# Optimization experiments

Measured on AMD Instinct MI355X. Metric: run time of the kernel, lower is better.

## Reference

```python
import jax, jax.numpy as jnp
from jax import lax
import numpy as np

IMG = 2048.0            # square image size (W=H)
STRIDES = [32, 64, 128]
FEATS = [64, 32, 16]    # IMG / stride
NUM_CLASSES = 80
BATCH = 8
SCORE_THRESH = 0.2
NMS_THRESH = 0.6
TOPK = 1000             # topk_candidates per level
DETS = 100              # detections_per_img


def make_anchors(fs, stride):
    # square anchors of size==stride centered on the feature grid (AnchorGenerator with ratio 1.0)
    c = (jnp.arange(fs, dtype=jnp.float32) + 0.5) * stride
    cy, cx = jnp.meshgrid(c, c, indexing='ij')
    cx, cy = cx.reshape(-1), cy.reshape(-1)
    h = stride / 2.0
    return jnp.stack([cx - h, cy - h, cx + h, cy + h], axis=1)


def setup_inputs() -> dict:
    key = jax.random.key(0)
    inp = {}
    for i, (fs, s) in enumerate(zip(FEATS, STRIDES)):
        hw = fs * fs
        key, k1, k2, k3 = jax.random.split(key, 4)
        inp[f'cls{i}'] = jax.random.normal(k1, (BATCH, hw, NUM_CLASSES), jnp.float32)
        inp[f'reg{i}'] = jax.random.uniform(k2, (BATCH, hw, 4), jnp.float32)
        inp[f'ctr{i}'] = jax.random.normal(k3, (BATCH, hw), jnp.float32)
        inp[f'anc{i}'] = make_anchors(fs, float(s))
    return inp


def _decode(rel, boxes):
    # BoxLinearCoder.decode_single with normalize_by_size=True
    cx = 0.5 * (boxes[:, 0] + boxes[:, 2])
    cy = 0.5 * (boxes[:, 1] + boxes[:, 3])
    w = boxes[:, 2] - boxes[:, 0]
    h = boxes[:, 3] - boxes[:, 1]
    rel = rel * jnp.stack([w, h, w, h], axis=1)
    return jnp.stack([cx - rel[:, 0], cy - rel[:, 1], cx + rel[:, 2], cy + rel[:, 3]], axis=1)


def _iou(b):
    # torchvision box_iou on a single set of boxes [N,4] -> [N,N]
    area = (b[:, 2] - b[:, 0]) * (b[:, 3] - b[:, 1])
    lt = jnp.maximum(b[:, None, :2], b[None, :, :2])
    rb = jnp.minimum(b[:, None, 2:], b[None, :, 2:])
    wh = jnp.clip(rb - lt, 0.0)
    inter = wh[..., 0] * wh[..., 1]
    return inter / (area[:, None] + area[None, :] - inter)


def _greedy_keep(iou):
    # classic greedy NMS on score-sorted boxes: suppress j>i with iou>thresh if i kept
    n = iou.shape[0]
    idx = jnp.arange(n)
    def body(i, keep):
        supp = keep[i] & (iou[i] > NMS_THRESH) & (idx > i)
        return keep & ~supp
    return lax.fori_loop(0, n, body, jnp.ones((n,), bool))


def _per_image(cls_l, reg_l, ctr_l, anc_l):
    boxes, scores, labels = [], [], []
    for cls, reg, ctr, anc in zip(cls_l, reg_l, ctr_l, anc_l):
        hw, c = cls.shape
        # scores = sqrt(sigmoid(cls) * sigmoid(ctrness)) flattened over anchors*classes
        sc = jnp.sqrt(jax.nn.sigmoid(cls) * jax.nn.sigmoid(ctr)[:, None]).reshape(-1)
        sc = jnp.where(sc > SCORE_THRESH, sc, -1.0)  # score threshold as mask (static shapes)
        ts, ti = lax.top_k(sc, TOPK)                 # per-level top-k candidates
        aidx = ti // c
        lab = ti % c
        b = jnp.clip(_decode(reg[aidx], anc[aidx]), 0.0, IMG)  # decode + clip to image
        boxes.append(b); scores.append(ts); labels.append(lab)
    boxes = jnp.concatenate(boxes)    # [3*TOPK, 4]
    scores = jnp.concatenate(scores)  # [3*TOPK]
    labels = jnp.concatenate(labels)  # [3*TOPK]
    n = scores.shape[0]
    # batched_nms via per-class coordinate offsets
    off = labels.astype(boxes.dtype) * (IMG + 1.0)
    ss, oi = lax.top_k(scores, n)     # sort candidates by score desc
    bs = boxes[oi] + off[oi][:, None]
    keep = lax.stop_gradient(_greedy_keep(_iou(bs)))
    fsc = jnp.where(keep & (ss > 0), ss, -1.0)
    fs, fi = lax.top_k(fsc, DETS)     # keep detections_per_img; score==-1 marks padding
    return boxes[oi][fi], fs, labels[oi][fi]


def reference(cls0, cls1, cls2, reg0, reg1, reg2, ctr0, ctr1, ctr2, anc0, anc1, anc2):
    f = jax.vmap(lambda c0, c1, c2, r0, r1, r2, t0, t1, t2: _per_image(
        [c0, c1, c2], [r0, r1, r2], [t0, t1, t2], [anc0, anc1, anc2]))
    return f(cls0, cls1, cls2, reg0, reg1, reg2, ctr0, ctr1, ctr2)
```

## Files before the change

### kernel.cpp

```cpp
#include <hip/hip_runtime.h>

#define NCLS  80
#define TOPK  384
#define SELK  512
#define NLVL  3
#define NIMG  8
#define NCAND (NLVL * TOPK)
#define DETS  100
#define CAP   1024
#define HBINS 4096
#define NHBLK 16
#define NCBLK 64
#define QBASE 0x3F800000u
#define QMAX  0x41C80000u
#define IMGSZ 2048.0f


__device__ __forceinline__ float sigm(float x) {
    if (x >= 0.f) return 1.f / (1.f + expf(-x));
    float e = expf(x);
    return e / (1.f + e);
}

__device__ __forceinline__ unsigned int qbits(float ea, float t1) {
    return __float_as_uint(__fmul_rn(__fadd_rn(1.f, ea), t1));
}

__device__ __forceinline__ void bitonic_desc(unsigned long long* s, int N) {
    for (int k = 2; k <= N; k <<= 1) {
        for (int j = k >> 1; j > 0; j >>= 1) {
            __syncthreads();
            for (int i = threadIdx.x; i < N; i += blockDim.x) {
                int ixj = i ^ j;
                if (ixj > i) {
                    unsigned long long a = s[i], b = s[ixj];
                    bool up = ((i & k) == 0);
                    if (up ? (a < b) : (a > b)) { s[i] = b; s[ixj] = a; }
                }
            }
        }
    }
    __syncthreads();
}

__device__ __forceinline__ void lvl_select(int level,
    const float* c0, const float* c1, const float* c2,
    const float* t0, const float* t1, const float* t2,
    const float** cls, const float** ctr, int* hw) {
    if (level == 0)      { *cls = c0; *ctr = t0; *hw = 4096; }
    else if (level == 1) { *cls = c1; *ctr = t1; *hw = 1024; }
    else                 { *cls = c2; *ctr = t2; *hw = 256; }
}


__global__ void k_hist(const float* c0, const float* c1, const float* c2,
                       const float* t0, const float* t1, const float* t2,
                       unsigned int* parts, unsigned int* counters) {
    int level = blockIdx.z, img = blockIdx.y;
    int pair = img * NLVL + level;
    if (blockIdx.x == 0 && threadIdx.x == 0) counters[pair * 16] = 0;
    const float* cls; const float* ctr; int hw;
    lvl_select(level, c0, c1, c2, t0, t1, t2, &cls, &ctr, &hw);
    int n4 = hw * (NCLS / 4);
    const float4* cl4 = (const float4*)(cls + (size_t)img * hw * NCLS);
    const float* ct = ctr + (size_t)img * hw;
    __shared__ unsigned int h[HBINS];
    for (int i = threadIdx.x; i < HBINS; i += 256) h[i] = 0;
    __syncthreads();
    for (int i = blockIdx.x * 256 + threadIdx.x; i < n4; i += NHBLK * 256) {
        float4 v = cl4[i];
        int a = i / (NCLS / 4);
        float eb = expf(-ct[a]);
        float t1 = __fadd_rn(1.f, eb);
        #pragma unroll
        for (int k = 0; k < 4; ++k) {
            float x = (k == 0) ? v.x : (k == 1) ? v.y : (k == 2) ? v.z : v.w;
            unsigned int qb = qbits(expf(-x), t1);
            if (qb < QMAX) {
                unsigned int bin = (qb - QBASE) >> 13;
                if (bin > HBINS - 1) bin = HBINS - 1;
                atomicAdd(&h[bin], 1u);
            }
        }
    }
    __syncthreads();
    unsigned int* P = parts + ((size_t)(pair * NHBLK + blockIdx.x)) * HBINS;
    for (int i = threadIdx.x; i < HBINS; i += 256) P[i] = h[i];
}


__global__ void k_find(const unsigned int* parts, unsigned int* vcut) {
    int pair = blockIdx.x;
    int tid = threadIdx.x;
    __shared__ unsigned int hb[HBINS];
    __shared__ unsigned int segsum[256];
    __shared__ unsigned int pref[256];
    unsigned int acc[HBINS / 256];
    #pragma unroll
    for (int j = 0; j < HBINS / 256; ++j) acc[j] = 0;
    for (int blk = 0; blk < NHBLK; ++blk) {
        const unsigned int* P = parts + ((size_t)(pair * NHBLK + blk)) * HBINS;
        #pragma unroll
        for (int j = 0; j < HBINS / 256; ++j) acc[j] += P[tid + 256 * j];
    }
    #pragma unroll
    for (int j = 0; j < HBINS / 256; ++j) hb[tid + 256 * j] = acc[j];
    __syncthreads();
    unsigned int seg = 0;
    #pragma unroll
    for (int j = 0; j < 16; ++j) seg += hb[16 * tid + j];
    segsum[tid] = seg;
    pref[tid] = seg;
    __syncthreads();
    for (int off = 1; off < 256; off <<= 1) {
        unsigned int v = (tid >= off) ? pref[tid - off] : 0u;
        __syncthreads();
        pref[tid] += v;
        __syncthreads();
    }
    unsigned int incl = pref[tid];
    unsigned int excl = incl - seg;
    if (excl < (unsigned int)SELK && incl >= (unsigned int)SELK) {
        unsigned int cum = excl; int B = HBINS - 1;
        for (int b = 16 * tid; b < 16 * tid + 16; ++b) {
            cum += hb[b];
            if (cum >= (unsigned int)SELK) { B = b; break; }
        }
        vcut[pair] = (B >= HBINS - 1) ? QMAX : (QBASE + ((unsigned int)(B + 1) << 13));
    }
    if (tid == 255 && pref[255] < (unsigned int)SELK)
        vcut[pair] = QMAX;
}


__global__ void k_collect(const float* c0, const float* c1, const float* c2,
                          const float* t0, const float* t1, const float* t2,
                          const unsigned int* vcut, unsigned int* counters,
                          unsigned long long* buf) {
    int level = blockIdx.z, img = blockIdx.y;
    const float* cls; const float* ctr; int hw;
    lvl_select(level, c0, c1, c2, t0, t1, t2, &cls, &ctr, &hw);
    int n4 = hw * (NCLS / 4);
    int pair = img * NLVL + level;
    const float4* cl4 = (const float4*)(cls + (size_t)img * hw * NCLS);
    const float* ct = ctr + (size_t)img * hw;
    unsigned int V = vcut[pair];
    __shared__ unsigned long long sbuf[CAP];
    __shared__ unsigned int scnt;
    __shared__ unsigned int sbase;
    if (threadIdx.x == 0) scnt = 0;
    __syncthreads();
    for (int i = blockIdx.x * 256 + threadIdx.x; i < n4; i += NCBLK * 256) {
        float4 v = cl4[i];
        int a = i / (NCLS / 4);
        float cta = ct[a];
        float eb = expf(-cta);
        float t1 = __fadd_rn(1.f, eb);
        #pragma unroll
        for (int k = 0; k < 4; ++k) {
            float x = (k == 0) ? v.x : (k == 1) ? v.y : (k == 2) ? v.z : v.w;
            unsigned int qb = qbits(expf(-x), t1);
            if (qb < V) {
                float s = sqrtf(sigm(x) * sigm(cta));
                unsigned int e = (unsigned int)(4 * i + k);
                unsigned int slot = atomicAdd(&scnt, 1u);
                if (slot < CAP)
                    sbuf[slot] = ((unsigned long long)__float_as_uint(s) << 32) | (~e);
            }
        }
    }
    __syncthreads();
    unsigned int cl_n = scnt; if (cl_n > CAP) cl_n = CAP;
    if (threadIdx.x == 0)
        sbase = atomicAdd(&counters[pair * 16], cl_n);
    __syncthreads();
    unsigned int base = sbase;
    for (unsigned int idx = threadIdx.x; idx < cl_n; idx += 256) {
        unsigned int g = base + idx;
        if (g < CAP) buf[(size_t)pair * CAP + g] = sbuf[idx];
    }
}


__global__ void __launch_bounds__(1024)
k_sort_pairs(const unsigned long long* buf, const unsigned int* counters,
             const float* r0, const float* r1, const float* r2,
             const float* a0, const float* a1, const float* a2,
             float* cand_box, int* cand_lab, unsigned long long* gkey) {
    int pair = blockIdx.x;
    int img = pair / NLVL, level = pair % NLVL;
    __shared__ unsigned long long s[CAP];
    int cnt = (int)counters[pair * 16]; if (cnt > CAP) cnt = CAP;
    for (int i = threadIdx.x; i < CAP; i += 1024)
        s[i] = (i < cnt) ? buf[(size_t)pair * CAP + i] : 0ull;
    bitonic_desc(s, CAP);
    const float* reg; const float* anc; int hw;
    if (level == 0)      { reg = r0; anc = a0; hw = 4096; }
    else if (level == 1) { reg = r1; anc = a1; hw = 1024; }
    else                 { reg = r2; anc = a2; hw = 256; }
    const float* rg = reg + (size_t)img * hw * 4;
    for (int r = threadIdx.x; r < TOPK; r += 1024) {
        unsigned long long key = s[r];
        int cpos = level * TOPK + r;
        size_t o = (size_t)img * NCAND + cpos;
        float b0 = 0, b1 = 0, b2 = 0, b3 = 0; int lab = 0; unsigned int bits = 0;
        if (key != 0ull) {
            bits = (unsigned int)(key >> 32);
            unsigned int idx = ~((unsigned int)key);
            int a = (int)(idx / NCLS); lab = (int)(idx % NCLS);
            float ax1 = anc[a * 4 + 0], ay1 = anc[a * 4 + 1];
            float ax2 = anc[a * 4 + 2], ay2 = anc[a * 4 + 3];
            float cx = 0.5f * (ax1 + ax2), cy = 0.5f * (ay1 + ay2);
            float w = ax2 - ax1, h = ay2 - ay1;
            float e0 = rg[a * 4 + 0] * w, e1 = rg[a * 4 + 1] * h;
            float e2 = rg[a * 4 + 2] * w, e3 = rg[a * 4 + 3] * h;
            b0 = fminf(fmaxf(cx - e0, 0.f), IMGSZ);
            b1 = fminf(fmaxf(cy - e1, 0.f), IMGSZ);
            b2 = fminf(fmaxf(cx + e2, 0.f), IMGSZ);
            b3 = fminf(fmaxf(cy + e3, 0.f), IMGSZ);
        }
        cand_box[o * 4 + 0] = b0; cand_box[o * 4 + 1] = b1;
        cand_box[o * 4 + 2] = b2; cand_box[o * 4 + 3] = b3;
        cand_lab[o] = lab;
        gkey[o] = ((unsigned long long)bits << 32) | (unsigned int)(~((unsigned int)cpos));
    }
}


__global__ void __launch_bounds__(1024)
k_merge_nms(const unsigned long long* gkey, const float* cand_box, const int* cand_lab,
            float* out) {
    int img = blockIdx.x;
    int tid = threadIdx.x;
    __shared__ unsigned long long A[TOPK], B[TOPK], C[TOPK];
    __shared__ unsigned long long M[2 * TOPK];
    __shared__ unsigned long long S[NCAND];
    __shared__ float4 wbox[NCAND];
    __shared__ int    wlab[NCAND];
    __shared__ float4 sbx[64]; __shared__ float sar[64];
    __shared__ float4 koff[DETS]; __shared__ float karr[DETS];
    __shared__ float4 kb[DETS]; __shared__ float ks[DETS]; __shared__ int kl[DETS];
    __shared__ float4 rb[DETS]; __shared__ int rl[DETS];

    const unsigned long long* G = gkey + (size_t)img * NCAND;
    for (int i = tid; i < TOPK; i += 1024) { A[i] = G[i]; B[i] = G[TOPK + i]; C[i] = G[2 * TOPK + i]; }
    __syncthreads();

    for (int k = tid; k < 2 * TOPK; k += 1024) {
        int lo = max(0, k - TOPK), hi = min(k, TOPK);
        while (lo < hi) {
            int mid = (lo + hi) >> 1;
            if (A[mid] > B[k - mid - 1]) lo = mid + 1; else hi = mid;
        }
        int i = lo, j = k - lo;
        unsigned long long av = (i < TOPK) ? A[i] : 0ull;
        unsigned long long bv = (j < TOPK) ? B[j] : 0ull;
        M[k] = (av > bv) ? av : bv;
    }
    __syncthreads();
    for (int k = tid; k < NCAND; k += 1024) {
        int lo = max(0, k - TOPK), hi = min(k, 2 * TOPK);
        while (lo < hi) {
            int mid = (lo + hi) >> 1;
            if (M[mid] > C[k - mid - 1]) lo = mid + 1; else hi = mid;
        }
        int i = lo, j = k - lo;
        unsigned long long mv = (i < 2 * TOPK) ? M[i] : 0ull;
        unsigned long long cv = (j < TOPK) ? C[j] : 0ull;
        S[k] = (mv > cv) ? mv : cv;
    }
    __syncthreads();

    const float4* CB4 = (const float4*)cand_box + (size_t)img * NCAND;
    const int* CL = cand_lab + (size_t)img * NCAND;
    for (int i = tid; i < NCAND; i += 1024) {
        unsigned int pos = ~((unsigned int)S[i]);
        float4 b4 = make_float4(0.f, 0.f, 0.f, 0.f); int lbv = 0;
        if (pos < NCAND) { b4 = CB4[pos]; lbv = CL[pos]; }
        wbox[i] = b4; wlab[i] = lbv;
    }
    __syncthreads();

    if (tid >= 64) return;
    int lane = tid;
    unsigned long long lmask_lt = (lane == 0) ? 0ull : (~0ull >> (64 - lane));

    int kept = 0, ring = 0, r = 0;

    while (kept < DETS && r < NCAND) {
        int rank = r + lane;
        unsigned long long key = (rank < NCAND) ? S[rank] : 0ull;
        unsigned int bits = (unsigned int)(key >> 32);
        unsigned long long pm = __ballot(bits != 0u);
        int npos = (pm == ~0ull) ? 64 : (int)__builtin_ctzll(~pm);
        if (npos == 0) break;

        float4 bx = make_float4(0.f, 0.f, 0.f, 0.f); int lb = 0;
        if (lane < npos) { bx = wbox[rank]; lb = wlab[rank]; }
        float off = (float)lb * (IMGSZ + 1.0f);
        float ox1 = bx.x + off, oy1 = bx.y + off;
        float ox2 = bx.z + off, oy2 = bx.w + off;
        float car = (ox2 - ox1) * (oy2 - oy1);
        sbx[lane] = make_float4(ox1, oy1, ox2, oy2);
        sar[lane] = car;

        bool supk = false;
        for (int k2 = 0; k2 < kept; ++k2) {
            float4 kk = koff[k2]; float ka = karr[k2];
            float lx = fmaxf(kk.x, ox1), ly = fmaxf(kk.y, oy1);
            float rx = fminf(kk.z, ox2), ry = fminf(kk.w, oy2);
            float w = fmaxf(rx - lx, 0.f), h = fmaxf(ry - ly, 0.f);
            float inter = w * h;
            supk = supk || (inter / (ka + car - inter) > 0.6f);
        }
        unsigned long long col = 0ull;
        for (int i = 0; i < npos; ++i) {
            float4 c = sbx[i]; float ca = sar[i];
            float lx = fmaxf(c.x, ox1), ly = fmaxf(c.y, oy1);
            float rx = fminf(c.z, ox2), ry = fminf(c.w, oy2);
            float w = fmaxf(rx - lx, 0.f), h = fmaxf(ry - ly, 0.f);
            float inter = w * h;
            if ((inter / (ca + car - inter) > 0.6f) && (i < lane)) col |= (1ull << i);
        }
        unsigned long long undecided = __ballot((lane < npos) && !supk);
        unsigned long long aliveSel = 0ull;
        int capleft = DETS - kept;
        int lastSlot = npos - 1;
        while (undecided) {
            int i = (int)__builtin_ctzll(undecided);
            aliveSel |= (1ull << i);
            undecided &= ~(1ull << i);
            if (--capleft == 0) { lastSlot = i; break; }
            unsigned long long row = __ballot(((col >> i) & 1ull) != 0ull);
            undecided &= ~row;
        }
        unsigned long long region = (lastSlot >= 63) ? ~0ull : ((1ull << (lastSlot + 1)) - 1ull);
        region &= (npos >= 64) ? ~0ull : ((1ull << npos) - 1ull);
        unsigned long long rejm = region & ~aliveSel;

        if ((aliveSel >> lane) & 1ull) {
            int ki = kept + (int)__popcll(aliveSel & lmask_lt);
            koff[ki] = make_float4(ox1, oy1, ox2, oy2); karr[ki] = car;
            kb[ki] = bx; ks[ki] = __uint_as_float(bits); kl[ki] = lb;
        }
        if ((rejm >> lane) & 1ull) {
            int ri = ring + (int)__popcll(rejm & lmask_lt);
            if (ri < DETS) { rb[ri] = bx; rl[ri] = lb; }
        }
        kept += (int)__popcll(aliveSel);
        ring += (int)__popcll(rejm);
        r += lastSlot + 1;
    }

    while (kept < DETS && ring < DETS && r < NCAND) {
        int rank = r + lane;
        if (rank < NCAND) {
            int ri = ring + lane;
            if (ri < DETS) { rb[ri] = wbox[rank]; rl[ri] = wlab[rank]; }
        }
        int take = NCAND - r; if (take > 64) take = 64;
        ring += take;
        r += 64;
    }

    for (int k = lane; k < DETS; k += 64) {
        float4 bxo; float scv; int lv;
        if (k < kept) { bxo = kb[k]; scv = ks[k]; lv = kl[k]; }
        else { int q = k - kept; bxo = rb[q]; scv = -1.0f; lv = rl[q]; }
        float* ob = out + ((size_t)img * DETS + k) * 4;
        ob[0] = bxo.x; ob[1] = bxo.y; ob[2] = bxo.z; ob[3] = bxo.w;
        out[NIMG * DETS * 4 + img * DETS + k] = scv;
        out[NIMG * DETS * 5 + img * DETS + k] = (float)lv;
    }
}


extern "C" void kernel_launch(void* const* d_in, const int* in_sizes, int n_in,
                              void* d_out, int out_size, void* d_ws, size_t ws_size,
                              hipStream_t stream) {
    (void)in_sizes; (void)n_in; (void)out_size; (void)ws_size;
    const float* cls0 = (const float*)d_in[0];
    const float* reg0 = (const float*)d_in[1];
    const float* ctr0 = (const float*)d_in[2];
    const float* anc0 = (const float*)d_in[3];
    const float* cls1 = (const float*)d_in[4];
    const float* reg1 = (const float*)d_in[5];
    const float* ctr1 = (const float*)d_in[6];
    const float* anc1 = (const float*)d_in[7];
    const float* cls2 = (const float*)d_in[8];
    const float* reg2 = (const float*)d_in[9];
    const float* ctr2 = (const float*)d_in[10];
    const float* anc2 = (const float*)d_in[11];
    float* out = (float*)d_out;
    char* ws = (char*)d_ws;

    const size_t OFF_PARTS = 0;
    const size_t OFF_CNT   = 6291456;
    const size_t OFF_VCUT  = 6292992;
    const size_t OFF_BUF   = 6293120;
    const size_t OFF_CBOX  = 6489728;
    const size_t OFF_CLAB  = 6637184;
    const size_t OFF_GKEY  = 6674048;

    unsigned int* parts = (unsigned int*)(ws + OFF_PARTS);
    unsigned int* cnt   = (unsigned int*)(ws + OFF_CNT);
    unsigned int* vcut  = (unsigned int*)(ws + OFF_VCUT);
    unsigned long long* buf  = (unsigned long long*)(ws + OFF_BUF);
    float* cand_box = (float*)(ws + OFF_CBOX);
    int*   cand_lab = (int*)(ws + OFF_CLAB);
    unsigned long long* gkey = (unsigned long long*)(ws + OFF_GKEY);

    k_hist<<<dim3(NHBLK, NIMG, NLVL), 256, 0, stream>>>(
        cls0, cls1, cls2, ctr0, ctr1, ctr2, parts, cnt);
    k_find<<<24, 256, 0, stream>>>(parts, vcut);
    k_collect<<<dim3(NCBLK, NIMG, NLVL), 256, 0, stream>>>(
        cls0, cls1, cls2, ctr0, ctr1, ctr2, vcut, cnt, buf);
    k_sort_pairs<<<24, 1024, 0, stream>>>(buf, cnt, reg0, reg1, reg2, anc0, anc1, anc2,
                                          cand_box, cand_lab, gkey);
    k_merge_nms<<<NIMG, 1024, 0, stream>>>(gkey, cand_box, cand_lab, out);
}
```

Before: 160.7 us.

## Fuse per-level sort and cross-level merge into one image-wide bitonic sort

Removes the separate per-(image,level) sort kernel and the global candidate staging buffers. The merge kernel now loads all three levels' collected keys for an image into a 4096-entry shared array, bitonic-sorts them together, and decodes boxes for the top 1024. The level is encoded into the key payload so decoding can recover it. This saves one launch and the global round trip plus merge-path searches, but runs a larger sort on only 8 blocks and changes the candidate set semantics from per-level top-k to global top-1024.

```diff
diff --git a/kernel.cpp b/kernel.cpp
--- a/kernel.cpp
+++ b/kernel.cpp
@@ -1,13 +1,13 @@
 #include <hip/hip_runtime.h>
 
 #define NCLS  80
-#define TOPK  384
 #define SELK  512
 #define NLVL  3
 #define NIMG  8
-#define NCAND (NLVL * TOPK)
 #define DETS  100
 #define CAP   1024
+#define NSORT 4096
+#define NDEC  1024
 #define HBINS 4096
 #define NHBLK 16
 #define NCBLK 64
@@ -163,9 +163,10 @@
             if (qb < V) {
                 float s = sqrtf(sigm(x) * sigm(cta));
                 unsigned int e = (unsigned int)(4 * i + k);
+                unsigned int p = ((unsigned int)level << 19) | e;
                 unsigned int slot = atomicAdd(&scnt, 1u);
                 if (slot < CAP)
-                    sbuf[slot] = ((unsigned long long)__float_as_uint(s) << 32) | (~e);
+                    sbuf[slot] = ((unsigned long long)__float_as_uint(s) << 32) | (~p);
             }
         }
     }
@@ -183,101 +184,55 @@
 
 
 __global__ void __launch_bounds__(1024)
-k_sort_pairs(const unsigned long long* buf, const unsigned int* counters,
-             const float* r0, const float* r1, const float* r2,
-             const float* a0, const float* a1, const float* a2,
-             float* cand_box, int* cand_lab, unsigned long long* gkey) {
-    int pair = blockIdx.x;
-    int img = pair / NLVL, level = pair % NLVL;
-    __shared__ unsigned long long s[CAP];
-    int cnt = (int)counters[pair * 16]; if (cnt > CAP) cnt = CAP;
-    for (int i = threadIdx.x; i < CAP; i += 1024)
-        s[i] = (i < cnt) ? buf[(size_t)pair * CAP + i] : 0ull;
-    bitonic_desc(s, CAP);
-    const float* reg; const float* anc; int hw;
-    if (level == 0)      { reg = r0; anc = a0; hw = 4096; }
-    else if (level == 1) { reg = r1; anc = a1; hw = 1024; }
-    else                 { reg = r2; anc = a2; hw = 256; }
-    const float* rg = reg + (size_t)img * hw * 4;
-    for (int r = threadIdx.x; r < TOPK; r += 1024) {
-        unsigned long long key = s[r];
-        int cpos = level * TOPK + r;
-        size_t o = (size_t)img * NCAND + cpos;
-        float b0 = 0, b1 = 0, b2 = 0, b3 = 0; int lab = 0; unsigned int bits = 0;
+k_merge_nms(const unsigned long long* buf, const unsigned int* counters,
+            const float* r0, const float* r1, const float* r2,
+            const float* a0, const float* a1, const float* a2,
+            float* out) {
+    int img = blockIdx.x;
+    int tid = threadIdx.x;
+    __shared__ unsigned long long S[NSORT];
+    __shared__ float4 wbox[NDEC];
+    __shared__ int    wlab[NDEC];
+    __shared__ float4 sbx[64]; __shared__ float sar[64];
+    __shared__ float4 koff[DETS]; __shared__ float karr[DETS];
+    __shared__ float4 kb[DETS]; __shared__ float ks[DETS]; __shared__ int kl[DETS];
+    __shared__ float4 rb[DETS]; __shared__ int rl[DETS];
+
+    for (int l = 0; l < NLVL; ++l) {
+        int pair = img * NLVL + l;
+        int c = (int)counters[pair * 16]; if (c > CAP) c = CAP;
+        const unsigned long long* B = buf + (size_t)pair * CAP;
+        for (int i = tid; i < CAP; i += 1024)
+            S[l * CAP + i] = (i < c) ? B[i] : 0ull;
+    }
+    for (int i = NLVL * CAP + tid; i < NSORT; i += 1024) S[i] = 0ull;
+    bitonic_desc(S, NSORT);
+
+    {
+        unsigned long long key = S[tid];
+        float4 b4 = make_float4(0.f, 0.f, 0.f, 0.f); int lbv = 0;
         if (key != 0ull) {
-            bits = (unsigned int)(key >> 32);
-            unsigned int idx = ~((unsigned int)key);
-            int a = (int)(idx / NCLS); lab = (int)(idx % NCLS);
+            unsigned int p = (~((unsigned int)key)) & 0x1FFFFFu;
+            int lvl = (int)(p >> 19);
+            unsigned int e = p & 0x7FFFFu;
+            int a = (int)(e / NCLS); lbv = (int)(e % NCLS);
+            const float* anc; const float* reg; int hw;
+            if (lvl == 0)      { anc = a0; reg = r0; hw = 4096; }
+            else if (lvl == 1) { anc = a1; reg = r1; hw = 1024; }
+            else               { anc = a2; reg = r2; hw = 256; }
+            const float* rg = reg + (size_t)img * hw * 4;
             float ax1 = anc[a * 4 + 0], ay1 = anc[a * 4 + 1];
             float ax2 = anc[a * 4 + 2], ay2 = anc[a * 4 + 3];
             float cx = 0.5f * (ax1 + ax2), cy = 0.5f * (ay1 + ay2);
             float w = ax2 - ax1, h = ay2 - ay1;
             float e0 = rg[a * 4 + 0] * w, e1 = rg[a * 4 + 1] * h;
             float e2 = rg[a * 4 + 2] * w, e3 = rg[a * 4 + 3] * h;
-            b0 = fminf(fmaxf(cx - e0, 0.f), IMGSZ);
-            b1 = fminf(fmaxf(cy - e1, 0.f), IMGSZ);
-            b2 = fminf(fmaxf(cx + e2, 0.f), IMGSZ);
-            b3 = fminf(fmaxf(cy + e3, 0.f), IMGSZ);
-        }
-        cand_box[o * 4 + 0] = b0; cand_box[o * 4 + 1] = b1;
-        cand_box[o * 4 + 2] = b2; cand_box[o * 4 + 3] = b3;
-        cand_lab[o] = lab;
-        gkey[o] = ((unsigned long long)bits << 32) | (unsigned int)(~((unsigned int)cpos));
-    }
-}
-
-
-__global__ void __launch_bounds__(1024)
-k_merge_nms(const unsigned long long* gkey, const float* cand_box, const int* cand_lab,
-            float* out) {
-    int img = blockIdx.x;
-    int tid = threadIdx.x;
-    __shared__ unsigned long long A[TOPK], B[TOPK], C[TOPK];
-    __shared__ unsigned long long M[2 * TOPK];
-    __shared__ unsigned long long S[NCAND];
-    __shared__ float4 wbox[NCAND];
-    __shared__ int    wlab[NCAND];
-    __shared__ float4 sbx[64]; __shared__ float sar[64];
-    __shared__ float4 koff[DETS]; __shared__ float karr[DETS];
-    __shared__ float4 kb[DETS]; __shared__ float ks[DETS]; __shared__ int kl[DETS];
-    __shared__ float4 rb[DETS]; __shared__ int rl[DETS];
-
-    const unsigned long long* G = gkey + (size_t)img * NCAND;
-    for (int i = tid; i < TOPK; i += 1024) { A[i] = G[i]; B[i] = G[TOPK + i]; C[i] = G[2 * TOPK + i]; }
-    __syncthreads();
-
-    for (int k = tid; k < 2 * TOPK; k += 1024) {
-        int lo = max(0, k - TOPK), hi = min(k, TOPK);
-        while (lo < hi) {
-            int mid = (lo + hi) >> 1;
-            if (A[mid] > B[k - mid - 1]) lo = mid + 1; else hi = mid;
-        }
-        int i = lo, j = k - lo;
-        unsigned long long av = (i < TOPK) ? A[i] : 0ull;
-        unsigned long long bv = (j < TOPK) ? B[j] : 0ull;
-        M[k] = (av > bv) ? av : bv;
-    }
-    __syncthreads();
-    for (int k = tid; k < NCAND; k += 1024) {
-        int lo = max(0, k - TOPK), hi = min(k, 2 * TOPK);
-        while (lo < hi) {
-            int mid = (lo + hi) >> 1;
-            if (M[mid] > C[k - mid - 1]) lo = mid + 1; else hi = mid;
-        }
-        int i = lo, j = k - lo;
-        unsigned long long mv = (i < 2 * TOPK) ? M[i] : 0ull;
-        unsigned long long cv = (j < TOPK) ? C[j] : 0ull;
-        S[k] = (mv > cv) ? mv : cv;
-    }
-    __syncthreads();
-
-    const float4* CB4 = (const float4*)cand_box + (size_t)img * NCAND;
-    const int* CL = cand_lab + (size_t)img * NCAND;
-    for (int i = tid; i < NCAND; i += 1024) {
-        unsigned int pos = ~((unsigned int)S[i]);
-        float4 b4 = make_float4(0.f, 0.f, 0.f, 0.f); int lbv = 0;
-        if (pos < NCAND) { b4 = CB4[pos]; lbv = CL[pos]; }
-        wbox[i] = b4; wlab[i] = lbv;
+            b4.x = fminf(fmaxf(cx - e0, 0.f), IMGSZ);
+            b4.y = fminf(fmaxf(cy - e1, 0.f), IMGSZ);
+            b4.z = fminf(fmaxf(cx + e2, 0.f), IMGSZ);
+            b4.w = fminf(fmaxf(cy + e3, 0.f), IMGSZ);
+        }
+        wbox[tid] = b4; wlab[tid] = lbv;
     }
     __syncthreads();
 
@@ -287,9 +242,9 @@
 
     int kept = 0, ring = 0, r = 0;
 
-    while (kept < DETS && r < NCAND) {
+    while (kept < DETS && r < NDEC) {
         int rank = r + lane;
-        unsigned long long key = (rank < NCAND) ? S[rank] : 0ull;
+        unsigned long long key = (rank < NDEC) ? S[rank] : 0ull;
         unsigned int bits = (unsigned int)(key >> 32);
         unsigned long long pm = __ballot(bits != 0u);
         int npos = (pm == ~0ull) ? 64 : (int)__builtin_ctzll(~pm);
@@ -352,13 +307,13 @@
         r += lastSlot + 1;
     }
 
-    while (kept < DETS && ring < DETS && r < NCAND) {
+    while (kept < DETS && ring < DETS && r < NDEC) {
         int rank = r + lane;
-        if (rank < NCAND) {
+        if (rank < NDEC) {
             int ri = ring + lane;
             if (ri < DETS) { rb[ri] = wbox[rank]; rl[ri] = wlab[rank]; }
         }
-        int take = NCAND - r; if (take > 64) take = 64;
+        int take = NDEC - r; if (take > 64) take = 64;
         ring += take;
         r += 64;
     }
@@ -398,24 +353,17 @@
     const size_t OFF_CNT   = 6291456;
     const size_t OFF_VCUT  = 6292992;
     const size_t OFF_BUF   = 6293120;
-    const size_t OFF_CBOX  = 6489728;
-    const size_t OFF_CLAB  = 6637184;
-    const size_t OFF_GKEY  = 6674048;
 
     unsigned int* parts = (unsigned int*)(ws + OFF_PARTS);
     unsigned int* cnt   = (unsigned int*)(ws + OFF_CNT);
     unsigned int* vcut  = (unsigned int*)(ws + OFF_VCUT);
     unsigned long long* buf  = (unsigned long long*)(ws + OFF_BUF);
-    float* cand_box = (float*)(ws + OFF_CBOX);
-    int*   cand_lab = (int*)(ws + OFF_CLAB);
-    unsigned long long* gkey = (unsigned long long*)(ws + OFF_GKEY);
 
     k_hist<<<dim3(NHBLK, NIMG, NLVL), 256, 0, stream>>>(
         cls0, cls1, cls2, ctr0, ctr1, ctr2, parts, cnt);
     k_find<<<24, 256, 0, stream>>>(parts, vcut);
     k_collect<<<dim3(NCBLK, NIMG, NLVL), 256, 0, stream>>>(
         cls0, cls1, cls2, ctr0, ctr1, ctr2, vcut, cnt, buf);
-    k_sort_pairs<<<24, 1024, 0, stream>>>(buf, cnt, reg0, reg1, reg2, anc0, anc1, anc2,
-                                          cand_box, cand_lab, gkey);
-    k_merge_nms<<<NIMG, 1024, 0, stream>>>(gkey, cand_box, cand_lab, out);
-}
+    k_merge_nms<<<NIMG, 1024, 0, stream>>>(buf, cnt, reg0, reg1, reg2,
+                                           anc0, anc1, anc2, out);
+}
```

Measured after the change: 195.3 us. +21.5%, slower.
